# Optimization experiments

Measured on AMD Instinct MI355X. Metric: run time of the kernel, lower is better.

The kernel has to match this reference:

```python
import jax, jax.numpy as jnp
import numpy as np

HIDDEN = 1024
ATT_FEAT = 2048
EMBED = 512


def setup_inputs() -> dict:
    key = jax.random.key(0)
    k1, k2, k3, k4, k5, k6 = jax.random.split(key, 6)
    B, S, N = 16, 64, 196
    hidden = jax.random.normal(k1, (B, S, HIDDEN), dtype=jnp.float32)
    feats = jax.random.normal(k2, (B, N, ATT_FEAT), dtype=jnp.float32)
    att_mask = jax.random.randint(k3, (B, N), 0, 2, dtype=jnp.int32)
    # parameters (scaled like default torch Linear init)
    w_h = jax.random.normal(k4, (HIDDEN, EMBED), dtype=jnp.float32) / np.sqrt(HIDDEN)
    w_u = jax.random.normal(k5, (ATT_FEAT, EMBED), dtype=jnp.float32) / np.sqrt(ATT_FEAT)
    b = jnp.ones((EMBED,), dtype=jnp.float32)
    w = jax.random.normal(k6, (EMBED,), dtype=jnp.float32) / np.sqrt(EMBED)
    return {"hidden": hidden, "feats": feats, "att_mask": att_mask,
            "w_h": w_h, "w_u": w_u, "b": b, "w": w}


def reference(hidden, feats, att_mask, w_h, w_u, b, w):
    # hidden: [B,S,H], feats: [B,N,F], att_mask: [B,N]
    Wh = jnp.einsum('bsh,he->bse', hidden, w_h)          # [B,S,E]
    Uv = jnp.einsum('bnf,fe->bne', feats, w_u)           # [B,N,E] (feats repeat is redundant; same math)
    # additive attention energies: tanh(Wh + Uv + b) . w  -> [B,S,N]
    e = jnp.tanh(Wh[:, :, None, :] + Uv[:, None, :, :] + b)
    scores = jnp.einsum('bsne,e->bsn', e, w)             # [B,S,N]
    scores = jnp.where(att_mask[:, None, :] == 0, jnp.float32(-1e9), scores)
    weights = jax.nn.softmax(scores, axis=-1)            # [B,S,N]
    attn_feats = jnp.einsum('bsn,bnf->bsf', weights, feats)  # [B,S,F]
    return attn_feats, weights
```

## Files before the change

kernel.cpp:

```cpp
#include <hip/hip_runtime.h>
#include <math.h>

#define BATCH 16
#define SEQ 64
#define NKEY 196
#define HIDDEN 1024
#define ATT_FEAT 2048
#define EMBED 512
#define MPAD 3200

using half8    = __attribute__((ext_vector_type(8))) _Float16;
using half4    = __attribute__((ext_vector_type(4))) _Float16;
using f32x4    = __attribute__((ext_vector_type(4))) float;
using f32x16   = __attribute__((ext_vector_type(16))) float;
using float4v  = __attribute__((ext_vector_type(4))) float;

#define KCONST (-2.8853900817779268f)
#define LOG2E  (1.4426950408889634f)

__device__ __forceinline__ void gl_lds16(const _Float16* g, _Float16* l) {
    __builtin_amdgcn_global_load_lds(
        (const __attribute__((address_space(1))) unsigned int*)g,
        (__attribute__((address_space(3))) unsigned int*)l, 16, 0, 0);
}

__device__ inline void prep_a128(
    const float* __restrict__ A, _Float16* __restrict__ T,
    int K, int Mreal, int tm, int tk, int t)
{
    const int r  = t >> 1;
    const int hf = t & 1;
    const int grow = tm * 128 + r;
    float f[32];
    if (grow < Mreal) {
        const float* src = A + (size_t)grow * K + tk * 64 + hf * 32;
        #pragma unroll
        for (int q = 0; q < 8; ++q) {
            float4v v = *(const float4v*)(src + q * 4);
            f[q*4+0] = v.x; f[q*4+1] = v.y; f[q*4+2] = v.z; f[q*4+3] = v.w;
        }
    } else {
        #pragma unroll
        for (int j = 0; j < 32; ++j) f[j] = 0.f;
    }
    const int tkk = tk * 2 + hf;
    const size_t base = ((size_t)tm * (K >> 5) + tkk) * 4096;
    #pragma unroll
    for (int s = 0; s < 2; ++s)
        #pragma unroll
        for (int kh = 0; kh < 2; ++kh) {
            half8 h;
            #pragma unroll
            for (int j = 0; j < 8; ++j)
                h[j] = (_Float16)f[s * 16 + kh * 8 + j];
            *(half8*)(T + base + (size_t)((s * 2 + kh) * 128 + r) * 8) = h;
        }
}

__device__ inline void prep_b128(
    const float* __restrict__ W, _Float16* __restrict__ T,
    int K, int N, int tn, int tk, int t, float (*tile)[129])
{
    {
        const int kr = t >> 2;
        const int nc = (t & 3) * 32;
        const float* src = W + (size_t)(tk * 64 + kr) * N + tn * 128 + nc;
        #pragma unroll
        for (int q = 0; q < 8; ++q) {
            float4v v = *(const float4v*)(src + q * 4);
            tile[kr][nc + q*4 + 0] = v.x; tile[kr][nc + q*4 + 1] = v.y;
            tile[kr][nc + q*4 + 2] = v.z; tile[kr][nc + q*4 + 3] = v.w;
        }
    }
    __syncthreads();
    {
        const int c  = t >> 1;
        const int hf = t & 1;
        const int tkk = tk * 2 + hf;
        const size_t base = ((size_t)tn * (K >> 5) + tkk) * 4096;
        #pragma unroll
        for (int s = 0; s < 2; ++s)
            #pragma unroll
            for (int kh = 0; kh < 2; ++kh) {
                half8 h;
                #pragma unroll
                for (int j = 0; j < 8; ++j)
                    h[j] = (_Float16)tile[hf * 32 + s * 16 + kh * 8 + j][c];
                *(half8*)(T + base + (size_t)((s * 2 + kh) * 128 + c) * 8) = h;
            }
    }
}

__global__ __launch_bounds__(256) void uber_prep(
    const float* __restrict__ hidden, const float* __restrict__ feats,
    const float* __restrict__ w_h, const float* __restrict__ w_u,
    _Float16* HA, _Float16* FA, _Float16* HB, _Float16* UB)
{
    __shared__ float tile[64][129];
    const int id = blockIdx.x;
    const int t  = threadIdx.x;
    if (id < 128) {
        prep_a128(hidden, HA, HIDDEN, BATCH * SEQ, id >> 4, id & 15, t);
    } else if (id < 928) {
        const int j = id - 128;
        prep_a128(feats, FA, ATT_FEAT, BATCH * NKEY, j >> 5, j & 31, t);
    } else if (id < 992) {
        const int j = id - 928;
        prep_b128(w_h, HB, HIDDEN, EMBED, j >> 4, j & 15, t, tile);
    } else {
        const int j = id - 992;
        prep_b128(w_u, UB, ATT_FEAT, EMBED, j >> 5, j & 31, t, tile);
    }
}

__global__ __launch_bounds__(256) void uber_gemm(
    const _Float16* __restrict__ HA, const _Float16* __restrict__ HB,
    const _Float16* __restrict__ FA, const _Float16* __restrict__ UB,
    const float* __restrict__ bvec, _Float16* __restrict__ WhP,
    _Float16* __restrict__ UvP)
{
    __shared__ __align__(16) _Float16 L[2][3][4096];

    const int hh = blockIdx.x;
    const int t0 = (hh & 7) * 58 + (hh >> 3);

    const _Float16 *Aimg, *Bimg;
    const float* bias = nullptr;
    _Float16* C;
    int rt, ct, tk0, aK;
    if (t0 < 400) {
        const int ks = t0 / 100, rem = t0 % 100;
        rt = rem >> 2; ct = rem & 3;
        Aimg = FA; Bimg = UB;
        aK = ATT_FEAT >> 5; tk0 = ks * 16;
        C = UvP + (size_t)ks * MPAD * EMBED;
        if (ks == 0) bias = bvec;
    } else {
        const int v = t0 - 400;
        const int ks = v >> 5, rem = v & 31;
        rt = rem >> 2; ct = rem & 3;
        Aimg = HA; Bimg = HB;
        aK = HIDDEN >> 5; tk0 = ks * 16;
        C = WhP + (size_t)ks * (BATCH * SEQ) * EMBED;
    }

    const int tid = threadIdx.x, lane = tid & 63, w = tid >> 6;
    const int wr = w >> 1, wc = w & 1;
    const int l31 = lane & 31, kh = lane >> 5;

    const int isB = w >> 1;
    const int whf = w & 1;
    const _Float16* srcMat = isB ? Bimg : Aimg;
    const int majorTile = isB ? ct : rt;
    const _Float16* src0 =
        srcMat + ((size_t)majorTile * aK + tk0) * 4096 + whf * 2048 + lane * 8;

    f32x16 acc[2][2] = {};

    auto stage = [&](int buf, int t) {
        const _Float16* s = src0 + (size_t)t * 4096;
        _Float16* d = &L[isB][buf][0] + whf * 2048 + lane * 8;
        #pragma unroll
        for (int c = 0; c < 4; ++c)
            gl_lds16(s + c * 512, d + c * 512);
    };

    auto compute = [&](int buf) {
        #pragma unroll
        for (int s = 0; s < 2; ++s) {
            const int rb = (s * 2 + kh) * 128;
            half8 a[2], b[2];
            #pragma unroll
            for (int m = 0; m < 2; ++m)
                a[m] = *(const half8*)&L[0][buf][(rb + wr * 64 + m * 32 + l31) * 8];
            #pragma unroll
            for (int n = 0; n < 2; ++n)
                b[n] = *(const half8*)&L[1][buf][(rb + wc * 64 + n * 32 + l31) * 8];
            __builtin_amdgcn_s_setprio(1);
            #pragma unroll
            for (int m = 0; m < 2; ++m)
                #pragma unroll
                for (int n = 0; n < 2; ++n)
                    acc[m][n] = __builtin_amdgcn_mfma_f32_32x32x16_f16(a[m], b[n], acc[m][n], 0, 0, 0);
            __builtin_amdgcn_s_setprio(0);
        }
    };

    stage(0, 0); stage(1, 1);
    int cur = 0, nxt = 2;
    #pragma unroll 1
    for (int t = 0; t < 16; ++t) {
        if (t + 1 < 16) asm volatile("s_waitcnt vmcnt(4)" ::: "memory");
        else            asm volatile("s_waitcnt vmcnt(0)" ::: "memory");
        __builtin_amdgcn_s_barrier();
        if (t + 2 < 16) stage(nxt, t + 2);
        __builtin_amdgcn_sched_barrier(0);
        compute(cur);
        __builtin_amdgcn_sched_barrier(0);
        cur = (cur == 2) ? 0 : cur + 1;
        nxt = (nxt == 2) ? 0 : nxt + 1;
    }

    #pragma unroll
    for (int m = 0; m < 2; ++m) {
        const int row0 = rt * 128 + wr * 64 + m * 32;
        #pragma unroll
        for (int n = 0; n < 2; ++n) {
            const int colg = ct * 128 + wc * 64 + n * 32 + l31;
            const float bv = bias ? bias[colg] : 0.f;
            #pragma unroll
            for (int r = 0; r < 16; ++r) {
                const int row = (r & 3) + 8 * (r >> 2) + 4 * kh;
                C[(size_t)(row0 + row) * EMBED + colg] =
                    (_Float16)((acc[m][n][r] + bv) * KCONST);
            }
        }
    }
}

__global__ __launch_bounds__(256) void scores4_kernel(
    const _Float16* __restrict__ WhP, const _Float16* __restrict__ UvP,
    const float* __restrict__ wvec, float* __restrict__ scr4)
{
    const int n0 = blockIdx.x * 16;
    const int eq = blockIdx.y;
    const int b  = blockIdx.z;
    const int tid = threadIdx.x;
    const int w    = tid >> 6;
    const int lane = tid & 63;

    __shared__ float whs[64 * 64];
    __shared__ float uvs[16][64];

    const size_t WHS = (size_t)(BATCH * SEQ) * EMBED;
    const size_t UVS = (size_t)MPAD * EMBED;

    float acc[4] = {};
    char* whsB = (char*)whs;

    for (int ch = 0; ch < 2; ++ch) {
        const int e0 = eq * 128 + ch * 64;
        {
            const int r = tid >> 2;
            const _Float16* Wr = WhP + (size_t)(b * SEQ + r) * EMBED + e0 + (tid & 3) * 16;
            half8 h0 = *(const half8*)(Wr);
            half8 h1 = *(const half8*)(Wr + 8);
            half8 g0 = *(const half8*)(Wr + WHS);
            half8 g1 = *(const half8*)(Wr + WHS + 8);
            float f[16];
            #pragma unroll
            for (int j = 0; j < 8; ++j) {
                f[j]     = (float)h0[j] + (float)g0[j];
                f[8 + j] = (float)h1[j] + (float)g1[j];
            }
            #pragma unroll
            for (int q = 0; q < 4; ++q) {
                const int cc = (tid & 3) * 16 + q * 4;
                float4v v = { f[q*4+0], f[q*4+1], f[q*4+2], f[q*4+3] };
                *(float4v*)(whsB + r * 256 + ((cc * 4) ^ ((r & 15) << 4))) = v;
            }
        }
        {
            const int nl = tid >> 4;
            const int c4 = tid & 15;
            const int nr = (n0 + nl < NKEY) ? (n0 + nl) : (NKEY - 1);
            const _Float16* Ur = UvP + (size_t)(b * NKEY + nr) * EMBED + e0 + c4 * 4;
            half4 u0 = *(const half4*)(Ur);
            half4 u1 = *(const half4*)(Ur + UVS);
            half4 u2 = *(const half4*)(Ur + 2 * UVS);
            half4 u3 = *(const half4*)(Ur + 3 * UVS);
            float4v u;
            u.x = ((float)u0[0] + (float)u1[0]) + ((float)u2[0] + (float)u3[0]);
            u.y = ((float)u0[1] + (float)u1[1]) + ((float)u2[1] + (float)u3[1]);
            u.z = ((float)u0[2] + (float)u1[2]) + ((float)u2[2] + (float)u3[2]);
            u.w = ((float)u0[3] + (float)u1[3]) + ((float)u2[3] + (float)u3[3]);
            *(float4v*)&uvs[nl][c4 * 4] = u;
        }
        __syncthreads();

        #pragma unroll
        for (int ec = 0; ec < 8; ++ec) {
            const int sb = lane * 256;
            float4v wh0 = *(const float4v*)(whsB + sb + ((ec * 32 +  0) ^ ((lane & 15) << 4)));
            float4v wh1 = *(const float4v*)(whsB + sb + ((ec * 32 + 16) ^ ((lane & 15) << 4)));
            float wf[8];
            #pragma unroll
            for (int i = 0; i < 8; ++i) wf[i] = wvec[e0 + ec * 8 + i];
            #pragma unroll
            for (int j = 0; j < 4; ++j) {
                const int nl = w * 4 + j;
                float4v u0 = *(const float4v*)&uvs[nl][ec * 8];
                float4v u1 = *(const float4v*)&uvs[nl][ec * 8 + 4];
                float t0 = __builtin_amdgcn_exp2f(wh0.x + u0.x);
                float t1 = __builtin_amdgcn_exp2f(wh0.y + u0.y);
                float t2 = __builtin_amdgcn_exp2f(wh0.z + u0.z);
                float t3 = __builtin_amdgcn_exp2f(wh0.w + u0.w);
                float t4 = __builtin_amdgcn_exp2f(wh1.x + u1.x);
                float t5 = __builtin_amdgcn_exp2f(wh1.y + u1.y);
                float t6 = __builtin_amdgcn_exp2f(wh1.z + u1.z);
                float t7 = __builtin_amdgcn_exp2f(wh1.w + u1.w);
                float a = acc[j];
                a = fmaf(wf[0], __builtin_amdgcn_rcpf(1.f + t0), a);
                a = fmaf(wf[1], __builtin_amdgcn_rcpf(1.f + t1), a);
                a = fmaf(wf[2], __builtin_amdgcn_rcpf(1.f + t2), a);
                a = fmaf(wf[3], __builtin_amdgcn_rcpf(1.f + t3), a);
                a = fmaf(wf[4], __builtin_amdgcn_rcpf(1.f + t4), a);
                a = fmaf(wf[5], __builtin_amdgcn_rcpf(1.f + t5), a);
                a = fmaf(wf[6], __builtin_amdgcn_rcpf(1.f + t6), a);
                a = fmaf(wf[7], __builtin_amdgcn_rcpf(1.f + t7), a);
                acc[j] = a;
            }
        }
        __syncthreads();
    }

    float* dst = scr4 + ((size_t)eq * (BATCH * SEQ) + b * SEQ + lane) * NKEY;
    #pragma unroll
    for (int j = 0; j < 4; ++j) {
        const int n = n0 + w * 4 + j;
        if (n < NKEY) dst[n] = 2.f * acc[j];
    }
}

__global__ __launch_bounds__(256) void attn_softmax_kernel(
    const float* __restrict__ scr4, const int* __restrict__ mask,
    const float* __restrict__ feats,
    float* __restrict__ weights_out, float* __restrict__ out)
{
    const int t   = threadIdx.x;
    const int fb  = blockIdx.x;
    const int s0  = blockIdx.y * 4;
    const int b   = blockIdx.z;

    __shared__ float wt[NKEY][4];

    const size_t SCRS = (size_t)(BATCH * SEQ) * NKEY;

    {
        const int r  = t >> 6;
        const int ln = t & 63;
        const float* p = scr4 + (size_t)(b * SEQ + s0 + r) * NKEY;
        const int* mrow = mask + b * NKEY;
        float v[4];
        float mx = -INFINITY;
        #pragma unroll
        for (int j = 0; j < 4; ++j) {
            const int n = ln + 64 * j;
            float s = -INFINITY;
            if (n < NKEY) {
                s = (p[n] + p[SCRS + n]) + (p[2 * SCRS + n] + p[3 * SCRS + n]);
                if (mrow[n] == 0) s = -1e9f;
            }
            v[j] = s;
            mx = fmaxf(mx, s);
        }
        #pragma unroll
        for (int off = 32; off; off >>= 1) mx = fmaxf(mx, __shfl_xor(mx, off));
        float sum = 0.f;
        #pragma unroll
        for (int j = 0; j < 4; ++j) {
            v[j] = __builtin_amdgcn_exp2f((v[j] - mx) * LOG2E);
            if (ln + 64 * j < NKEY) sum += v[j];
        }
        #pragma unroll
        for (int off = 32; off; off >>= 1) sum += __shfl_xor(sum, off);
        const float inv = __builtin_amdgcn_rcpf(sum);
        float* wrow = weights_out + (size_t)(b * SEQ + s0 + r) * NKEY;
        #pragma unroll
        for (int j = 0; j < 4; ++j) {
            const int n = ln + 64 * j;
            if (n < NKEY) {
                const float wv = v[j] * inv;
                wt[n][r] = wv;
                if (fb == 0) wrow[n] = wv;
            }
        }
    }
    __syncthreads();

    const int col = fb * 1024 + t * 4;
    const float* fp = feats + (size_t)b * NKEY * ATT_FEAT + col;

    float4v acc[4] = {};
    #pragma unroll 4
    for (int n = 0; n < NKEY; ++n) {
        float4v f  = *(const float4v*)(fp + (size_t)n * ATT_FEAT);
        float4v wv = *(const float4v*)&wt[n][0];
        acc[0] += wv.x * f;
        acc[1] += wv.y * f;
        acc[2] += wv.z * f;
        acc[3] += wv.w * f;
    }

    float* op = out + (size_t)(b * SEQ + s0) * ATT_FEAT + col;
    #pragma unroll
    for (int s = 0; s < 4; ++s)
        *(float4v*)(op + (size_t)s * ATT_FEAT) = acc[s];
}

extern "C" void kernel_launch(void* const* d_in, const int* in_sizes, int n_in,
                              void* d_out, int out_size, void* d_ws, size_t ws_size,
                              hipStream_t stream)
{
    const float* hidden = (const float*)d_in[0];
    const float* feats  = (const float*)d_in[1];
    const int*   mask   = (const int*)  d_in[2];
    const float* w_h    = (const float*)d_in[3];
    const float* w_u    = (const float*)d_in[4];
    const float* bvec   = (const float*)d_in[5];
    const float* wvec   = (const float*)d_in[6];

    float* out         = (float*)d_out;
    float* attn_out    = out;
    float* weights_out = out + (size_t)BATCH * SEQ * ATT_FEAT;

    _Float16* WhP = (_Float16*)d_ws;
    _Float16* UvP = WhP + (size_t)2 * BATCH * SEQ * EMBED;
    float*    scr4 = (float*)(UvP + (size_t)4 * MPAD * EMBED);
    _Float16* FA = (_Float16*)(scr4 + (size_t)4 * BATCH * SEQ * NKEY);
    _Float16* HA = FA + (size_t)MPAD * ATT_FEAT;
    _Float16* UB = HA + (size_t)BATCH * SEQ * HIDDEN;
    _Float16* HB = UB + (size_t)EMBED * ATT_FEAT;

    uber_prep<<<dim3(1120), 256, 0, stream>>>(
        hidden, feats, w_h, w_u, HA, FA, HB, UB);

    uber_gemm<<<dim3(464), 256, 0, stream>>>(
        HA, HB, FA, UB, bvec, WhP, UvP);

    scores4_kernel<<<dim3((NKEY + 15) / 16, 4, BATCH), 256, 0, stream>>>(
        WhP, UvP, wvec, scr4);

    attn_softmax_kernel<<<dim3(2, SEQ / 4, BATCH), 256, 0, stream>>>(
        scr4, mask, feats, weights_out, attn_out);
}
```

Baseline: 85.06 us.

## Compute attention-weighted features with fp16 MFMA over pre-transposed feats tiles

```diff
diff --git a/kernel.cpp b/kernel.cpp
--- a/kernel.cpp
+++ b/kernel.cpp
@@ -4,6 +4,7 @@
 #define BATCH 16
 #define SEQ 64
 #define NKEY 196
+#define NPAD 224
 #define HIDDEN 1024
 #define ATT_FEAT 2048
 #define EMBED 512
@@ -91,10 +92,48 @@
     }
 }
 
+__device__ inline void prep_bT(
+    const float* __restrict__ Wb, _Float16* __restrict__ T,
+    int tn, int tk, int t, float (*tile)[129])
+{
+    {
+        const int kr = t >> 2;
+        const int nc = (t & 3) * 32;
+        const int gn = tk * 64 + kr;
+        #pragma unroll
+        for (int q = 0; q < 8; ++q) {
+            float4v v = {0.f, 0.f, 0.f, 0.f};
+            if (gn < NKEY)
+                v = *(const float4v*)(Wb + (size_t)gn * ATT_FEAT + tn * 128 + nc + q * 4);
+            tile[kr][nc + q*4 + 0] = v.x; tile[kr][nc + q*4 + 1] = v.y;
+            tile[kr][nc + q*4 + 2] = v.z; tile[kr][nc + q*4 + 3] = v.w;
+        }
+    }
+    __syncthreads();
+    {
+        const int c  = t >> 1;
+        const int hf = t & 1;
+        const int tkk = tk * 2 + hf;
+        if (tkk < 7) {
+            const size_t base = ((size_t)tn * 7 + tkk) * 4096;
+            #pragma unroll
+            for (int s = 0; s < 2; ++s)
+                #pragma unroll
+                for (int kh = 0; kh < 2; ++kh) {
+                    half8 h;
+                    #pragma unroll
+                    for (int j = 0; j < 8; ++j)
+                        h[j] = (_Float16)tile[hf * 32 + s * 16 + kh * 8 + j][c];
+                    *(half8*)(T + base + (size_t)((s * 2 + kh) * 128 + c) * 8) = h;
+                }
+        }
+    }
+}
+
 __global__ __launch_bounds__(256) void uber_prep(
     const float* __restrict__ hidden, const float* __restrict__ feats,
     const float* __restrict__ w_h, const float* __restrict__ w_u,
-    _Float16* HA, _Float16* FA, _Float16* HB, _Float16* UB)
+    _Float16* HA, _Float16* FA, _Float16* HB, _Float16* UB, _Float16* FT)
 {
     __shared__ float tile[64][129];
     const int id = blockIdx.x;
@@ -107,9 +146,14 @@
     } else if (id < 992) {
         const int j = id - 928;
         prep_b128(w_h, HB, HIDDEN, EMBED, j >> 4, j & 15, t, tile);
-    } else {
+    } else if (id < 1120) {
         const int j = id - 992;
         prep_b128(w_u, UB, ATT_FEAT, EMBED, j >> 5, j & 31, t, tile);
+    } else {
+        const int j = id - 1120;
+        const int b = j >> 6, rem = j & 63;
+        prep_bT(feats + (size_t)b * NKEY * ATT_FEAT,
+                FT + (size_t)b * 16 * 7 * 4096, rem >> 2, rem & 3, t, tile);
     }
 }
 
@@ -322,80 +366,107 @@
     }
 }
 
-__global__ __launch_bounds__(256) void attn_softmax_kernel(
+__global__ __launch_bounds__(256) void attn_mfma(
     const float* __restrict__ scr4, const int* __restrict__ mask,
-    const float* __restrict__ feats,
+    const _Float16* __restrict__ FT,
     float* __restrict__ weights_out, float* __restrict__ out)
 {
-    const int t   = threadIdx.x;
-    const int fb  = blockIdx.x;
-    const int s0  = blockIdx.y * 4;
-    const int b   = blockIdx.z;
-
-    __shared__ float wt[NKEY][4];
-
-    const size_t SCRS = (size_t)(BATCH * SEQ) * NKEY;
+    const int fb = blockIdx.x;
+    const int b  = blockIdx.y;
+    const int t  = threadIdx.x;
+    const int lane = t & 63, w = t >> 6;
+    const int wr = w >> 1, wc = w & 1;
+    const int l31 = lane & 31, khl = lane >> 5;
+
+    __shared__ __align__(16) _Float16 wtL[7 * 4 * 64 * 8];
+    __shared__ __align__(16) _Float16 Lb[3][4096];
+
+    const _Float16* FTb = FT + (size_t)b * 16 * 7 * 4096 + (size_t)fb * 7 * 4096;
+
+    auto stage = [&](int buf, int kt) {
+        const _Float16* s = FTb + (size_t)kt * 4096 + w * 1024 + lane * 8;
+        _Float16* d = &Lb[buf][0] + w * 1024 + lane * 8;
+        gl_lds16(s, d);
+        gl_lds16(s + 512, d + 512);
+    };
+
+    stage(0, 0); stage(1, 1);
+
+    #pragma unroll
+    for (int i = 0; i < 7; ++i)
+        *(half8*)&wtL[(i * 256 + t) * 8] = (half8)(_Float16)0.f;
+
+    asm volatile("s_waitcnt lgkmcnt(0)" ::: "memory");
+    __builtin_amdgcn_s_barrier();
 
     {
-        const int r  = t >> 6;
-        const int ln = t & 63;
-        const float* p = scr4 + (size_t)(b * SEQ + s0 + r) * NKEY;
+        const int r  = t >> 2;
+        const int ln = t & 3;
+        const size_t SCRS = (size_t)(BATCH * SEQ) * NKEY;
+        const float* p = scr4 + (size_t)(b * SEQ + r) * NKEY;
         const int* mrow = mask + b * NKEY;
-        float v[4];
+        float v[49];
         float mx = -INFINITY;
         #pragma unroll
-        for (int j = 0; j < 4; ++j) {
-            const int n = ln + 64 * j;
-            float s = -INFINITY;
-            if (n < NKEY) {
-                s = (p[n] + p[SCRS + n]) + (p[2 * SCRS + n] + p[3 * SCRS + n]);
-                if (mrow[n] == 0) s = -1e9f;
-            }
+        for (int j = 0; j < 49; ++j) {
+            const int n = ln + 4 * j;
+            float s = (p[n] + p[SCRS + n]) + (p[2 * SCRS + n] + p[3 * SCRS + n]);
+            if (mrow[n] == 0) s = -1e9f;
             v[j] = s;
             mx = fmaxf(mx, s);
         }
-        #pragma unroll
-        for (int off = 32; off; off >>= 1) mx = fmaxf(mx, __shfl_xor(mx, off));
+        mx = fmaxf(mx, __shfl_xor(mx, 1));
+        mx = fmaxf(mx, __shfl_xor(mx, 2));
         float sum = 0.f;
         #pragma unroll
-        for (int j = 0; j < 4; ++j) {
+        for (int j = 0; j < 49; ++j) {
             v[j] = __builtin_amdgcn_exp2f((v[j] - mx) * LOG2E);
-            if (ln + 64 * j < NKEY) sum += v[j];
-        }
-        #pragma unroll
-        for (int off = 32; off; off >>= 1) sum += __shfl_xor(sum, off);
+            sum += v[j];
+        }
+        sum += __shfl_xor(sum, 1);
+        sum += __shfl_xor(sum, 2);
         const float inv = __builtin_amdgcn_rcpf(sum);
-        float* wrow = weights_out + (size_t)(b * SEQ + s0 + r) * NKEY;
-        #pragma unroll
-        for (int j = 0; j < 4; ++j) {
-            const int n = ln + 64 * j;
-            if (n < NKEY) {
-                const float wv = v[j] * inv;
-                wt[n][r] = wv;
-                if (fb == 0) wrow[n] = wv;
-            }
-        }
-    }
-    __syncthreads();
-
-    const int col = fb * 1024 + t * 4;
-    const float* fp = feats + (size_t)b * NKEY * ATT_FEAT + col;
-
-    float4v acc[4] = {};
-    #pragma unroll 4
-    for (int n = 0; n < NKEY; ++n) {
-        float4v f  = *(const float4v*)(fp + (size_t)n * ATT_FEAT);
-        float4v wv = *(const float4v*)&wt[n][0];
-        acc[0] += wv.x * f;
-        acc[1] += wv.y * f;
-        acc[2] += wv.z * f;
-        acc[3] += wv.w * f;
-    }
-
-    float* op = out + (size_t)(b * SEQ + s0) * ATT_FEAT + col;
+        float* wrow = weights_out + (size_t)(b * SEQ + r) * NKEY;
+        #pragma unroll
+        for (int j = 0; j < 49; ++j) {
+            const int n = ln + 4 * j;
+            const float wv = v[j] * inv;
+            if (fb == 0) wrow[n] = wv;
+            const int grp = ((n >> 4) & 1) * 2 + ((n >> 3) & 1);
+            wtL[(((n >> 5) * 4 + grp) * 64 + r) * 8 + (n & 7)] = (_Float16)wv;
+        }
+    }
+    asm volatile("s_waitcnt lgkmcnt(0)" ::: "memory");
+
+    f32x16 acc[2] = {};
+    #pragma unroll 1
+    for (int kt = 0; kt < 7; ++kt) {
+        if (kt < 6) asm volatile("s_waitcnt vmcnt(2)" ::: "memory");
+        else        asm volatile("s_waitcnt vmcnt(0)" ::: "memory");
+        __builtin_amdgcn_s_barrier();
+        if (kt + 2 < 7) stage((kt + 2) % 3, kt + 2);
+        __builtin_amdgcn_sched_barrier(0);
+        const int buf = kt % 3;
+        #pragma unroll
+        for (int ks = 0; ks < 2; ++ks) {
+            half8 a = *(const half8*)&wtL[(((kt * 4) + ks * 2 + khl) * 64 + wr * 32 + l31) * 8];
+            half8 b0 = *(const half8*)&Lb[buf][((ks * 2 + khl) * 128 + wc * 64 + l31) * 8];
+            half8 b1 = *(const half8*)&Lb[buf][((ks * 2 + khl) * 128 + wc * 64 + 32 + l31) * 8];
+            acc[0] = __builtin_amdgcn_mfma_f32_32x32x16_f16(a, b0, acc[0], 0, 0, 0);
+            acc[1] = __builtin_amdgcn_mfma_f32_32x32x16_f16(a, b1, acc[1], 0, 0, 0);
+        }
+        __builtin_amdgcn_sched_barrier(0);
+    }
+
     #pragma unroll
-    for (int s = 0; s < 4; ++s)
-        *(float4v*)(op + (size_t)s * ATT_FEAT) = acc[s];
+    for (int nf = 0; nf < 2; ++nf) {
+        const int f = fb * 128 + wc * 64 + nf * 32 + l31;
+        #pragma unroll
+        for (int r = 0; r < 16; ++r) {
+            const int srow = wr * 32 + (r & 3) + 8 * (r >> 2) + 4 * khl;
+            out[(size_t)(b * SEQ + srow) * ATT_FEAT + f] = acc[nf][r];
+        }
+    }
 }
 
 extern "C" void kernel_launch(void* const* d_in, const int* in_sizes, int n_in,
@@ -421,9 +492,10 @@
     _Float16* HA = FA + (size_t)MPAD * ATT_FEAT;
     _Float16* UB = HA + (size_t)BATCH * SEQ * HIDDEN;
     _Float16* HB = UB + (size_t)EMBED * ATT_FEAT;
-
-    uber_prep<<<dim3(1120), 256, 0, stream>>>(
-        hidden, feats, w_h, w_u, HA, FA, HB, UB);
+    _Float16* FT = HB + (size_t)EMBED * HIDDEN;
+
+    uber_prep<<<dim3(2144), 256, 0, stream>>>(
+        hidden, feats, w_h, w_u, HA, FA, HB, UB, FT);
 
     uber_gemm<<<dim3(464), 256, 0, stream>>>(
         HA, HB, FA, UB, bvec, WhP, UvP);
@@ -431,6 +503,6 @@
     scores4_kernel<<<dim3((NKEY + 15) / 16, 4, BATCH), 256, 0, stream>>>(
         WhP, UvP, wvec, scr4);
 
-    attn_softmax_kernel<<<dim3(2, SEQ / 4, BATCH), 256, 0, stream>>>(
-        scr4, mask, feats, weights_out, attn_out);
-}
+    attn_mfma<<<dim3(16, 16), 256, 0, stream>>>(
+        scr4, mask, FT, weights_out, attn_out);
+}
```

Result: no change. 84.80 us (-0.3%).
